# Kernel tuning notes

Measured on AMD Instinct MI355X. Metric: run time of the kernel, lower is better.

## Reference

```python
import jax, jax.numpy as jnp
import numpy as np

N_JOINTS = 18

_RELATIVE_JOINT_MAP = np.array([[0,3,2,1,3,3,3,3,3,3,3,3,3,3,3,3,3,3],[3,0,2,3,1,1,3,3,3,3,2,3,2,2,2,3,3,3],[2,2,0,1,1,3,3,3,1,2,2,3,3,3,3,3,3,3],[1,3,1,0,2,3,3,3,2,3,3,3,3,3,3,3,3,3],[3,1,1,2,0,2,3,2,2,3,1,3,3,3,3,3,3,3],[3,1,3,3,2,0,3,3,3,3,3,3,1,1,1,3,3,3],[3,3,3,3,3,3,0,3,2,1,3,3,3,3,3,3,3,3],[3,3,3,3,2,3,3,0,2,3,1,1,3,3,3,2,2,2],[3,3,1,2,2,3,2,2,0,1,1,3,3,3,3,3,3,3],[3,3,2,3,3,3,1,3,1,0,2,3,3,3,3,3,3,3],[3,2,2,3,1,3,3,1,1,2,0,2,3,3,3,3,3,3],[3,3,3,3,3,3,3,1,3,3,2,0,3,3,3,1,1,1],[3,2,3,3,3,1,3,3,3,3,3,3,0,1,2,3,3,3],[3,2,3,3,3,1,3,3,3,3,3,3,1,0,2,3,3,3],[3,2,3,3,3,1,3,3,3,3,3,3,2,2,0,3,3,3],[3,3,3,3,3,3,3,2,3,3,3,1,3,3,3,0,1,2],[3,3,3,3,3,3,3,2,3,3,3,1,3,3,3,1,0,2],[3,3,3,3,3,3,3,2,3,3,3,1,3,3,3,2,2,0]], dtype=np.int32)

DIM = 512
HEADS = 8
DEPTH = DIM // HEADS  # 64
BATCH = 4096


def setup_inputs() -> dict:
    key = jax.random.key(0)
    ks = jax.random.split(key, 10)
    std = 0.02
    return {
        "k": jax.random.normal(ks[0], (BATCH, N_JOINTS, DIM), jnp.float32),
        "v": jax.random.normal(ks[1], (BATCH, N_JOINTS, DIM), jnp.float32),
        "q": jax.random.normal(ks[2], (BATCH, N_JOINTS, DIM), jnp.float32),
        "Wq": jax.random.normal(ks[3], (DIM, DIM), jnp.float32) * (DIM ** -0.5),
        "Wk": jax.random.normal(ks[4], (DIM, DIM), jnp.float32) * (DIM ** -0.5),
        "Wv": jax.random.normal(ks[5], (DIM, DIM), jnp.float32) * (DIM ** -0.5),
        "Wo": jax.random.normal(ks[6], (DIM, DIM), jnp.float32) * (DIM ** -0.5),
        "bo": jnp.zeros((DIM,), jnp.float32),
        "rel_k": jax.random.normal(ks[7], (4, DEPTH), jnp.float32) * std,
        "rel_v": jax.random.normal(ks[8], (4, DEPTH), jnp.float32) * std,
        "joint_map": jnp.asarray(_RELATIVE_JOINT_MAP),
    }


def reference(k, v, q, Wq, Wk, Wv, Wo, bo, rel_k, rel_v, joint_map):
    B, n, dim = q.shape
    h, d = HEADS, DEPTH
    scale = d ** -0.5

    def split_heads(x):  # [B, n, h*d] -> [B, h, n, d]
        return x.reshape(B, n, h, d).transpose(0, 2, 1, 3)

    qh = split_heads(q @ Wq)
    kh = split_heads(k @ Wk)
    vh = split_heads(v @ Wv)

    # gather relative position tables: [n, n, d]
    r_pos_k = rel_k[joint_map]
    r_pos_v = rel_v[joint_map]

    # relative bias sums over heads AND depth of K (faithful to original einsum)
    rel_bias = jnp.einsum('bhid,ijd->bij', kh, r_pos_k)  # [B, n, n]
    dots = (jnp.einsum('bhid,bhjd->bhij', qh, kh) + rel_bias[:, None, :, :]) * scale
    att = jax.nn.softmax(dots, axis=-1)  # [B, h, n, n]

    out = jnp.einsum('bhij,bhjd->bhid', att, vh) + jnp.einsum('bhij,ijd->bhid', att, r_pos_v)
    out = out.transpose(0, 2, 1, 3).reshape(B, n, dim)
    out = out @ Wo + bo
    return out, att
```

## Files before the change

kernel.cpp:

```cpp
#include <hip/hip_runtime.h>
#include <stdint.h>

#define BATCH 4096
#define NJ 18
#define DIMM 512
#define HEADS 8
#define DEPTH 64
#define MROWS (BATCH*NJ)
#define ATT_OFF ((size_t)MROWS*DIMM)

typedef float f32x4 __attribute__((ext_vector_type(4)));
typedef _Float16 f16_t;
typedef _Float16 f16x8 __attribute__((ext_vector_type(8)));

__device__ __forceinline__ void gl_lds16(const unsigned int* g, unsigned int* l) {
    __builtin_amdgcn_global_load_lds(g, l, 16, 0, 0);
}

__global__ __launch_bounds__(256) void convert_w_kernel(
    const float* __restrict__ W0, const float* __restrict__ W1,
    const float* __restrict__ W2, const float* __restrict__ W3,
    f16_t* __restrict__ T0, f16_t* __restrict__ T1,
    f16_t* __restrict__ T2, f16_t* __restrict__ T3)
{
    const float* W = blockIdx.z == 0 ? W0 : blockIdx.z == 1 ? W1 : blockIdx.z == 2 ? W2 : W3;
    f16_t* T       = blockIdx.z == 0 ? T0 : blockIdx.z == 1 ? T1 : blockIdx.z == 2 ? T2 : T3;
    __shared__ float ld[64][65];
    int k0 = blockIdx.y * 64, n0 = blockIdx.x * 64;
    int tid = threadIdx.x;
    #pragma unroll
    for (int it = 0; it < 16; ++it) {
        int idx = tid + it * 256;
        int kk = idx >> 6, nn = idx & 63;
        ld[kk][nn] = W[(size_t)(k0 + kk) * DIMM + n0 + nn];
    }
    __syncthreads();
    f16x8* T8 = (f16x8*)T;
    #pragma unroll
    for (int it = 0; it < 2; ++it) {
        int c = tid + it * 256;
        int nn = c >> 3, c8 = c & 7;
        int n = n0 + nn, k = k0 + c8 * 8;
        f16x8 val;
        #pragma unroll
        for (int e = 0; e < 8; ++e) val[e] = (f16_t)ld[c8 * 8 + e][nn];
        size_t vi = (size_t)((n >> 7) * 8 + (k >> 6)) * 1024
                  + (n & 127) * 8 + (((k >> 3) & 7) ^ (n & 7));
        T8[vi] = val;
    }
}

template <int MODE>
__global__ __launch_bounds__(256) void gemm16_kernel(
    const void* __restrict__ A0, const void* __restrict__ A1,
    const void* __restrict__ A2,
    const f16_t* __restrict__ B0, const f16_t* __restrict__ B1,
    const f16_t* __restrict__ B2,
    void* __restrict__ C0, void* __restrict__ C1, void* __restrict__ C2,
    const float* __restrict__ bias)
{
    const void* Aparm = blockIdx.z == 0 ? A0 : blockIdx.z == 1 ? A1 : A2;
    const f16_t* Bt   = blockIdx.z == 0 ? B0 : blockIdx.z == 1 ? B1 : B2;
    void* Cparm       = blockIdx.z == 0 ? C0 : blockIdx.z == 1 ? C1 : C2;

    const int p = blockIdx.x + 4 * blockIdx.y;
    const int logical = (p & 7) * (2304 / 8) + (p >> 3);
    const int bn = (logical & 3) * 128;
    const int bm = (logical >> 2) * 128;

    __shared__ __align__(16) f16_t As[MODE == 0 ? 128 * 72 : 128 * 64];
    __shared__ __align__(16) f16_t Bs[128 * 64];

    const int tid = threadIdx.x;
    const int lane = tid & 63;
    const int wv = tid >> 6;
    const int wm = wv >> 1, wn = wv & 1;
    const int l15 = lane & 15, lg = lane >> 4;
    const int swz = (l15 & 7) << 4;
    const int koffb[2] = { (lg * 16) ^ swz, (lg * 16 + 64) ^ swz };

    f32x4 acc[4][4] = {};

    for (int ks = 0; ks < 8; ++ks) {
        __syncthreads();
        {
            const unsigned int* btile =
                (const unsigned int*)(Bt + (size_t)((bn >> 7) * 8 + ks) * 8192);
            unsigned int* bs = (unsigned int*)Bs;
            #pragma unroll
            for (int it = 0; it < 4; ++it) {
                int chunk = wv * 4 + it;
                gl_lds16(btile + chunk * 256 + lane * 4, bs + chunk * 256);
            }
        }
        if constexpr (MODE == 0) {
            const float* A = (const float*)Aparm;
            #pragma unroll
            for (int r = 0; r < 4; ++r) {
                int c = tid + r * 256;
                int row = c >> 3, kc = c & 7;
                const f32x4* p4 = (const f32x4*)(A + (size_t)(bm + row) * DIMM + ks * 64 + kc * 8);
                f32x4 a0 = p4[0], a1 = p4[1];
                f16x8 val;
                val[0] = (f16_t)a0[0]; val[1] = (f16_t)a0[1];
                val[2] = (f16_t)a0[2]; val[3] = (f16_t)a0[3];
                val[4] = (f16_t)a1[0]; val[5] = (f16_t)a1[1];
                val[6] = (f16_t)a1[2]; val[7] = (f16_t)a1[3];
                *(f16x8*)(&As[row * 72 + kc * 8]) = val;
            }
        } else {
            const unsigned int* atile =
                (const unsigned int*)((const f16_t*)Aparm + (size_t)((bm >> 7) * 8 + ks) * 8192);
            unsigned int* as = (unsigned int*)As;
            #pragma unroll
            for (int it = 0; it < 4; ++it) {
                int chunk = wv * 4 + it;
                gl_lds16(atile + chunk * 256 + lane * 4, as + chunk * 256);
            }
        }
        __syncthreads();

        #pragma unroll
        for (int kk = 0; kk < 2; ++kk) {
            const int koff = koffb[kk];
            f16x8 af[4], bfr[4];
            #pragma unroll
            for (int mi = 0; mi < 4; ++mi) {
                int row = wm * 64 + mi * 16 + l15;
                if constexpr (MODE == 0)
                    af[mi] = *(const f16x8*)(&As[row * 72 + kk * 32 + lg * 8]);
                else
                    af[mi] = *(const f16x8*)((const char*)As + row * 128 + koff);
            }
            #pragma unroll
            for (int ni = 0; ni < 4; ++ni) {
                int row = wn * 64 + ni * 16 + l15;
                bfr[ni] = *(const f16x8*)((const char*)Bs + row * 128 + koff);
            }
            #pragma unroll
            for (int mi = 0; mi < 4; ++mi)
                #pragma unroll
                for (int ni = 0; ni < 4; ++ni)
                    acc[mi][ni] = __builtin_amdgcn_mfma_f32_16x16x32_f16(
                        af[mi], bfr[ni], acc[mi][ni], 0, 0, 0);
        }
    }

    #pragma unroll
    for (int mi = 0; mi < 4; ++mi) {
        #pragma unroll
        for (int ni = 0; ni < 4; ++ni) {
            int col = bn + wn * 64 + ni * 16 + l15;
            int rowb = bm + wm * 64 + mi * 16 + lg * 4;
            f32x4 v = acc[mi][ni];
            if constexpr (MODE == 1) {
                float* C = (float*)Cparm;
                float bv = bias[col];
                #pragma unroll
                for (int r = 0; r < 4; ++r)
                    C[(size_t)(rowb + r) * DIMM + col] = v[r] + bv;
            } else {
                f16_t* C = (f16_t*)Cparm;
                #pragma unroll
                for (int r = 0; r < 4; ++r)
                    C[(size_t)(rowb + r) * DIMM + col] = (f16_t)v[r];
            }
        }
    }
}

__global__ __launch_bounds__(256, 3) void attn_kernel(
    const f16_t* __restrict__ qh, const f16_t* __restrict__ kh,
    const f16_t* __restrict__ vh,
    const float* __restrict__ rel_k, const float* __restrict__ rel_v,
    const int* __restrict__ jmap,
    float* __restrict__ att_out, f16_t* __restrict__ ao)
{
    const int b = blockIdx.x;
    const int tid = threadIdx.x;
    __shared__ __align__(16) f16_t k_s[NJ * DIMM];
    __shared__ __align__(16) f16_t v_s[NJ * DIMM];
    __shared__ float relk_s[4 * DEPTH];
    __shared__ float relv_s[4 * DEPTH];
    __shared__ int map_s[NJ * NJ];
    __shared__ float ksum_s[NJ * DEPTH];
    __shared__ float t4_s[NJ * 4];

    const size_t base = (size_t)b * (NJ * DIMM);
    const uint4* kg = (const uint4*)(kh + base);
    const uint4* vg = (const uint4*)(vh + base);
    uint4* ks4 = (uint4*)k_s;
    uint4* vs4 = (uint4*)v_s;
    for (int c = tid; c < 2 * NJ * 64; c += 256) {
        int t = c / (NJ * 64);
        int e = c - t * (NJ * 64);
        int m = e & 63;
        int pos = (e & ~63) + (m & 56) + (((m & 7) + (m >> 3)) & 7);
        uint4 val = (t == 0 ? kg : vg)[e];
        (t == 0 ? ks4 : vs4)[pos] = val;
    }
    relk_s[tid & 255] = rel_k[tid & 255];
    relv_s[tid & 255] = rel_v[tid & 255];
    for (int e = tid; e < NJ * NJ; e += 256) map_s[e] = jmap[e];

    const int h = tid / NJ, i = tid - (tid / NJ) * NJ;
    const bool act = tid < HEADS * NJ;
    f16x8 qr[8];
    if (act) {
        const f16x8* qp = (const f16x8*)(qh + base + i * DIMM + h * DEPTH);
        #pragma unroll
        for (int t = 0; t < 8; ++t) qr[t] = qp[t];
    }
    __syncthreads();

    const f16x8* ks8 = (const f16x8*)k_s;
    const f16x8* vs8 = (const f16x8*)v_s;

    for (int e = tid; e < NJ * DEPTH; e += 256) {
        int ii = e >> 6, dd = e & 63;
        int tt = dd >> 3, d7 = dd & 7;
        float s = 0.f;
        #pragma unroll
        for (int hh = 0; hh < HEADS; ++hh)
            s += (float)k_s[((ii << 6) + (hh << 3) + ((tt + hh) & 7)) * 8 + d7];
        ksum_s[e] = s;
    }
    __syncthreads();
    if (tid < NJ * 4) {
        int ii = tid >> 2, c = tid & 3;
        float s = 0.f;
        #pragma unroll
        for (int dd = 0; dd < DEPTH; ++dd)
            s += ksum_s[ii * DEPTH + dd] * relk_s[c * DEPTH + dd];
        t4_s[tid] = s;
    }
    __syncthreads();

    if (!act) return;

    float att[NJ];
    float m = -1e30f;
    #pragma unroll
    for (int j = 0; j < NJ; ++j) {
        float s = 0.f;
        #pragma unroll
        for (int t = 0; t < 8; ++t) {
            f16x8 kv = ks8[(j << 6) + (h << 3) + ((t + h) & 7)];
            f16x8 a = qr[t];
            #pragma unroll
            for (int e = 0; e < 8; ++e) s += (float)a[e] * (float)kv[e];
        }
        s += t4_s[i * 4 + map_s[i * NJ + j]];
        s *= 0.125f;
        att[j] = s;
        m = fmaxf(m, s);
    }
    float sum = 0.f;
    #pragma unroll
    for (int j = 0; j < NJ; ++j) { att[j] = __expf(att[j] - m); sum += att[j]; }
    const float inv = 1.f / sum;
    float s4[4] = {0.f, 0.f, 0.f, 0.f};
    float* ap = att_out + (((size_t)b * HEADS + h) * NJ + i) * NJ;
    #pragma unroll
    for (int j = 0; j < NJ; ++j) {
        float a = att[j] * inv;
        att[j] = a;
        ap[j] = a;
        int c = map_s[i * NJ + j];
        s4[0] += (c == 0) ? a : 0.f;
        s4[1] += (c == 1) ? a : 0.f;
        s4[2] += (c == 2) ? a : 0.f;
        s4[3] += (c == 3) ? a : 0.f;
    }

    const size_t grow = (size_t)b * NJ + i;
    f16x8* aot = (f16x8*)ao + ((grow >> 7) * 8 + h) * 1024 + (grow & 127) * 8;
    const int rr7 = (int)(grow & 7);
    #pragma unroll
    for (int half = 0; half < 2; ++half) {
        float acc[32] = {};
        #pragma unroll
        for (int j = 0; j < NJ; ++j) {
            float a = att[j];
            #pragma unroll
            for (int t = 0; t < 4; ++t) {
                int tt = half * 4 + t;
                f16x8 vv = vs8[(j << 6) + (h << 3) + ((tt + h) & 7)];
                #pragma unroll
                for (int e = 0; e < 8; ++e) acc[t * 8 + e] += a * (float)vv[e];
            }
        }
        #pragma unroll
        for (int c = 0; c < 4; ++c) {
            float sc = s4[c];
            #pragma unroll
            for (int d = 0; d < 32; ++d)
                acc[d] += sc * relv_s[c * DEPTH + half * 32 + d];
        }
        #pragma unroll
        for (int t = 0; t < 4; ++t) {
            f16x8 res;
            #pragma unroll
            for (int e = 0; e < 8; ++e) res[e] = (f16_t)acc[t * 8 + e];
            aot[(half * 4 + t) ^ rr7] = res;
        }
    }
}

extern "C" void kernel_launch(void* const* d_in, const int* in_sizes, int n_in,
                              void* d_out, int out_size, void* d_ws, size_t ws_size,
                              hipStream_t stream) {
    (void)in_sizes; (void)n_in; (void)out_size; (void)ws_size;
    const float* k_in = (const float*)d_in[0];
    const float* v_in = (const float*)d_in[1];
    const float* q_in = (const float*)d_in[2];
    const float* Wq   = (const float*)d_in[3];
    const float* Wk   = (const float*)d_in[4];
    const float* Wv   = (const float*)d_in[5];
    const float* Wo   = (const float*)d_in[6];
    const float* bo   = (const float*)d_in[7];
    const float* relk = (const float*)d_in[8];
    const float* relv = (const float*)d_in[9];
    const int*   jmap = (const int*)d_in[10];

    char* ws = (char*)d_ws;
    const size_t WT = (size_t)DIMM * DIMM * sizeof(f16_t);
    f16_t* Tq = (f16_t*)(ws + 0 * WT);
    f16_t* Tk = (f16_t*)(ws + 1 * WT);
    f16_t* Tv = (f16_t*)(ws + 2 * WT);
    f16_t* To = (f16_t*)(ws + 3 * WT);
    const size_t PSZ = (size_t)MROWS * DIMM * sizeof(f16_t);
    f16_t* qh = (f16_t*)(ws + 4 * WT + 0 * PSZ);
    f16_t* kh = (f16_t*)(ws + 4 * WT + 1 * PSZ);
    f16_t* vh = (f16_t*)(ws + 4 * WT + 2 * PSZ);
    f16_t* ao = (f16_t*)(ws + 4 * WT + 3 * PSZ);

    float* outp = (float*)d_out;
    float* attp = outp + ATT_OFF;

    convert_w_kernel<<<dim3(8, 8, 4), 256, 0, stream>>>(
        Wq, Wk, Wv, Wo, Tq, Tk, Tv, To);

    gemm16_kernel<0><<<dim3(DIMM / 128, MROWS / 128, 3), 256, 0, stream>>>(
        q_in, k_in, v_in, Tq, Tk, Tv, qh, kh, vh, nullptr);

    attn_kernel<<<BATCH, 256, 0, stream>>>(qh, kh, vh, relk, relv, jmap, attp, ao);

    gemm16_kernel<1><<<dim3(DIMM / 128, MROWS / 128, 1), 256, 0, stream>>>(
        ao, nullptr, nullptr, To, nullptr, nullptr, outp, nullptr, nullptr, bo);
}
```

Measured before the change: 447.8 us.

## Double-buffer B tile in LDS and load A fragments directly into registers

The GEMM kernel drops the A shared-memory tile. Each wave now loads its A fragments straight from global memory into registers, converting fp32 to fp16 in registers for MODE 0 or reading the pre-swizzled fp16 image for MODE 1. The B tile is double-buffered in LDS, and the next k-step is prefetched with global_load_lds before the current MFMAs run, using hand-placed vmcnt waits and barriers. The aim is to overlap global loads with compute and cut LDS traffic and one barrier per k-step. In exchange it relies on fragile hand-counted vmcnt values and on uncoalesced per-lane A reads in MODE 0, where the second half of each A step is loaded late without prefetch.

```diff
diff --git a/kernel.cpp b/kernel.cpp
--- a/kernel.cpp
+++ b/kernel.cpp
@@ -68,8 +68,7 @@
     const int bn = (logical & 3) * 128;
     const int bm = (logical >> 2) * 128;
 
-    __shared__ __align__(16) f16_t As[MODE == 0 ? 128 * 72 : 128 * 64];
-    __shared__ __align__(16) f16_t Bs[128 * 64];
+    __shared__ __align__(16) f16_t Bs[2][128 * 64];
 
     const int tid = threadIdx.x;
     const int lane = tid & 63;
@@ -79,63 +78,91 @@
     const int swz = (l15 & 7) << 4;
     const int koffb[2] = { (lg * 16) ^ swz, (lg * 16 + 64) ^ swz };
 
+    const float* arow = (const float*)Aparm
+        + (size_t)(bm + wm * 64 + l15) * DIMM + lg * 8;
+    const f16x8* aimg = (const f16x8*)Aparm
+        + (size_t)(bm >> 7) * 8 * 1024 + (wm * 64 + l15) * 8;
+    const int axor = l15 & 7;
+
     f32x4 acc[4][4] = {};
 
+    auto stageB = [&](int ks, int buf) {
+        const unsigned int* btile =
+            (const unsigned int*)(Bt + (size_t)((bn >> 7) * 8 + ks) * 8192);
+        unsigned int* bs = (unsigned int*)(&Bs[buf][0]);
+        #pragma unroll
+        for (int it = 0; it < 4; ++it) {
+            int chunk = wv * 4 + it;
+            gl_lds16(btile + chunk * 256 + lane * 4, bs + chunk * 256);
+        }
+    };
+
+    stageB(0, 0);
+
     for (int ks = 0; ks < 8; ++ks) {
-        __syncthreads();
-        {
-            const unsigned int* btile =
-                (const unsigned int*)(Bt + (size_t)((bn >> 7) * 8 + ks) * 8192);
-            unsigned int* bs = (unsigned int*)Bs;
-            #pragma unroll
-            for (int it = 0; it < 4; ++it) {
-                int chunk = wv * 4 + it;
-                gl_lds16(btile + chunk * 256 + lane * 4, bs + chunk * 256);
-            }
-        }
+        const int buf = ks & 1;
+
+        f32x4 a0p[4], a1p[4];
+        f16x8 afp[8];
         if constexpr (MODE == 0) {
-            const float* A = (const float*)Aparm;
-            #pragma unroll
-            for (int r = 0; r < 4; ++r) {
-                int c = tid + r * 256;
-                int row = c >> 3, kc = c & 7;
-                const f32x4* p4 = (const f32x4*)(A + (size_t)(bm + row) * DIMM + ks * 64 + kc * 8);
-                f32x4 a0 = p4[0], a1 = p4[1];
-                f16x8 val;
-                val[0] = (f16_t)a0[0]; val[1] = (f16_t)a0[1];
-                val[2] = (f16_t)a0[2]; val[3] = (f16_t)a0[3];
-                val[4] = (f16_t)a1[0]; val[5] = (f16_t)a1[1];
-                val[6] = (f16_t)a1[2]; val[7] = (f16_t)a1[3];
-                *(f16x8*)(&As[row * 72 + kc * 8]) = val;
+            #pragma unroll
+            for (int mi = 0; mi < 4; ++mi) {
+                const f32x4* ap = (const f32x4*)(arow + (size_t)mi * 16 * DIMM + ks * 64);
+                a0p[mi] = ap[0];
+                a1p[mi] = ap[1];
             }
         } else {
-            const unsigned int* atile =
-                (const unsigned int*)((const f16_t*)Aparm + (size_t)((bm >> 7) * 8 + ks) * 8192);
-            unsigned int* as = (unsigned int*)As;
-            #pragma unroll
-            for (int it = 0; it < 4; ++it) {
-                int chunk = wv * 4 + it;
-                gl_lds16(atile + chunk * 256 + lane * 4, as + chunk * 256);
-            }
-        }
-        __syncthreads();
+            #pragma unroll
+            for (int kk = 0; kk < 2; ++kk)
+                #pragma unroll
+                for (int mi = 0; mi < 4; ++mi)
+                    afp[kk * 4 + mi] = aimg[ks * 1024 + mi * 128 + ((kk * 4 + lg) ^ axor)];
+        }
+
+        if (ks < 7) stageB(ks + 1, buf ^ 1);
+
+        if (ks < 7) asm volatile("s_waitcnt vmcnt(12)" ::: "memory");
+        else        asm volatile("s_waitcnt vmcnt(8)"  ::: "memory");
+        __builtin_amdgcn_s_barrier();
+        __builtin_amdgcn_sched_barrier(0);
 
         #pragma unroll
         for (int kk = 0; kk < 2; ++kk) {
             const int koff = koffb[kk];
             f16x8 af[4], bfr[4];
-            #pragma unroll
-            for (int mi = 0; mi < 4; ++mi) {
-                int row = wm * 64 + mi * 16 + l15;
-                if constexpr (MODE == 0)
-                    af[mi] = *(const f16x8*)(&As[row * 72 + kk * 32 + lg * 8]);
-                else
-                    af[mi] = *(const f16x8*)((const char*)As + row * 128 + koff);
+            if constexpr (MODE == 0) {
+                if (kk == 0) {
+                    #pragma unroll
+                    for (int mi = 0; mi < 4; ++mi) {
+                        f32x4 a0 = a0p[mi], a1 = a1p[mi];
+                        f16x8 v;
+                        v[0] = (f16_t)a0[0]; v[1] = (f16_t)a0[1];
+                        v[2] = (f16_t)a0[2]; v[3] = (f16_t)a0[3];
+                        v[4] = (f16_t)a1[0]; v[5] = (f16_t)a1[1];
+                        v[6] = (f16_t)a1[2]; v[7] = (f16_t)a1[3];
+                        af[mi] = v;
+                    }
+                } else {
+                    #pragma unroll
+                    for (int mi = 0; mi < 4; ++mi) {
+                        const f32x4* ap = (const f32x4*)(arow + (size_t)mi * 16 * DIMM + ks * 64 + 32);
+                        f32x4 a0 = ap[0], a1 = ap[1];
+                        f16x8 v;
+                        v[0] = (f16_t)a0[0]; v[1] = (f16_t)a0[1];
+                        v[2] = (f16_t)a0[2]; v[3] = (f16_t)a0[3];
+                        v[4] = (f16_t)a1[0]; v[5] = (f16_t)a1[1];
+                        v[6] = (f16_t)a1[2]; v[7] = (f16_t)a1[3];
+                        af[mi] = v;
+                    }
+                }
+            } else {
+                #pragma unroll
+                for (int mi = 0; mi < 4; ++mi) af[mi] = afp[kk * 4 + mi];
             }
             #pragma unroll
             for (int ni = 0; ni < 4; ++ni) {
                 int row = wn * 64 + ni * 16 + l15;
-                bfr[ni] = *(const f16x8*)((const char*)Bs + row * 128 + koff);
+                bfr[ni] = *(const f16x8*)((const char*)(&Bs[buf][0]) + row * 128 + koff);
             }
             #pragma unroll
             for (int mi = 0; mi < 4; ++mi)
@@ -144,6 +171,9 @@
                     acc[mi][ni] = __builtin_amdgcn_mfma_f32_16x16x32_f16(
                         af[mi], bfr[ni], acc[mi][ni], 0, 0, 0);
         }
+
+        asm volatile("s_waitcnt lgkmcnt(0)" ::: "memory");
+        __builtin_amdgcn_s_barrier();
     }
 
     #pragma unroll
```

New measurement: 714.9 us. 59.6% more time.

## Software-pipeline fp32 A loads and double-buffer B tiles in QKV GEMM

Applied to the files above, without the earlier changes.

In the MODE 0 GEMM (fp32 activations converted to fp16), the loop now issues the next k-step's A register loads and B global-to-LDS copies before computing on the current step. B lives in a double-buffered LDS array, and synchronisation uses manual waitcnt plus scheduling barriers. The goal is to hide global memory latency behind the MFMA work. The cost is more registers for prefetched A, twice the LDS for B, and hand-tuned waitcnt counts that must match the number of outstanding loads. MODE 1 behaves as before.

```diff
diff --git a/kernel.cpp b/kernel.cpp
--- a/kernel.cpp
+++ b/kernel.cpp
@@ -16,6 +16,9 @@
 __device__ __forceinline__ void gl_lds16(const unsigned int* g, unsigned int* l) {
     __builtin_amdgcn_global_load_lds(g, l, 16, 0, 0);
 }
+#define SBAR()  do { __builtin_amdgcn_sched_barrier(0); \
+                     __builtin_amdgcn_s_barrier();      \
+                     __builtin_amdgcn_sched_barrier(0); } while (0)
 
 __global__ __launch_bounds__(256) void convert_w_kernel(
     const float* __restrict__ W0, const float* __restrict__ W1,
@@ -69,7 +72,7 @@
     const int bm = (logical >> 2) * 128;
 
     __shared__ __align__(16) f16_t As[MODE == 0 ? 128 * 72 : 128 * 64];
-    __shared__ __align__(16) f16_t Bs[128 * 64];
+    __shared__ __align__(16) f16_t Bs[MODE == 0 ? 2 * 128 * 64 : 128 * 64];
 
     const int tid = threadIdx.x;
     const int lane = tid & 63;
@@ -81,68 +84,128 @@
 
     f32x4 acc[4][4] = {};
 
-    for (int ks = 0; ks < 8; ++ks) {
-        __syncthreads();
-        {
-            const unsigned int* btile =
-                (const unsigned int*)(Bt + (size_t)((bn >> 7) * 8 + ks) * 8192);
-            unsigned int* bs = (unsigned int*)Bs;
-            #pragma unroll
-            for (int it = 0; it < 4; ++it) {
-                int chunk = wv * 4 + it;
-                gl_lds16(btile + chunk * 256 + lane * 4, bs + chunk * 256);
-            }
-        }
-        if constexpr (MODE == 0) {
-            const float* A = (const float*)Aparm;
+    auto stageB = [&](int ks, int buf) {
+        const unsigned int* btile =
+            (const unsigned int*)(Bt + (size_t)((bn >> 7) * 8 + ks) * 8192);
+        unsigned int* bs = (unsigned int*)(&Bs[0]) + buf * 4096;
+        #pragma unroll
+        for (int it = 0; it < 4; ++it) {
+            int chunk = wv * 4 + it;
+            gl_lds16(btile + chunk * 256 + lane * 4, bs + chunk * 256);
+        }
+    };
+
+    if constexpr (MODE == 0) {
+        const int kc = tid & 7;
+        const int rw0 = tid >> 3;
+        const float* abase[4];
+        #pragma unroll
+        for (int r = 0; r < 4; ++r)
+            abase[r] = (const float*)Aparm + (size_t)(bm + rw0 + r * 32) * DIMM + kc * 8;
+
+        f32x4 apre[8];
+        #pragma unroll
+        for (int r = 0; r < 4; ++r) {
+            const f32x4* ap = (const f32x4*)(abase[r]);
+            apre[r * 2]     = ap[0];
+            apre[r * 2 + 1] = ap[1];
+        }
+        stageB(0, 0);
+
+        #pragma unroll
+        for (int ks = 0; ks < 8; ++ks) {
+            const int buf = ks & 1;
+
+            f16x8 vals[4];
             #pragma unroll
             for (int r = 0; r < 4; ++r) {
-                int c = tid + r * 256;
-                int row = c >> 3, kc = c & 7;
-                const f32x4* p4 = (const f32x4*)(A + (size_t)(bm + row) * DIMM + ks * 64 + kc * 8);
-                f32x4 a0 = p4[0], a1 = p4[1];
-                f16x8 val;
-                val[0] = (f16_t)a0[0]; val[1] = (f16_t)a0[1];
-                val[2] = (f16_t)a0[2]; val[3] = (f16_t)a0[3];
-                val[4] = (f16_t)a1[0]; val[5] = (f16_t)a1[1];
-                val[6] = (f16_t)a1[2]; val[7] = (f16_t)a1[3];
-                *(f16x8*)(&As[row * 72 + kc * 8]) = val;
-            }
-        } else {
-            const unsigned int* atile =
-                (const unsigned int*)((const f16_t*)Aparm + (size_t)((bm >> 7) * 8 + ks) * 8192);
-            unsigned int* as = (unsigned int*)As;
-            #pragma unroll
-            for (int it = 0; it < 4; ++it) {
-                int chunk = wv * 4 + it;
-                gl_lds16(atile + chunk * 256 + lane * 4, as + chunk * 256);
-            }
-        }
-        __syncthreads();
-
-        #pragma unroll
-        for (int kk = 0; kk < 2; ++kk) {
-            const int koff = koffb[kk];
-            f16x8 af[4], bfr[4];
-            #pragma unroll
-            for (int mi = 0; mi < 4; ++mi) {
-                int row = wm * 64 + mi * 16 + l15;
-                if constexpr (MODE == 0)
+                f32x4 a0 = apre[r * 2], a1 = apre[r * 2 + 1];
+                f16x8 v;
+                v[0] = (f16_t)a0[0]; v[1] = (f16_t)a0[1];
+                v[2] = (f16_t)a0[2]; v[3] = (f16_t)a0[3];
+                v[4] = (f16_t)a1[0]; v[5] = (f16_t)a1[1];
+                v[6] = (f16_t)a1[2]; v[7] = (f16_t)a1[3];
+                vals[r] = v;
+            }
+            #pragma unroll
+            for (int r = 0; r < 4; ++r)
+                *(f16x8*)(&As[(rw0 + r * 32) * 72 + kc * 8]) = vals[r];
+
+            if (ks < 7) {
+                #pragma unroll
+                for (int r = 0; r < 4; ++r) {
+                    const f32x4* ap = (const f32x4*)(abase[r] + (ks + 1) * 64);
+                    apre[r * 2]     = ap[0];
+                    apre[r * 2 + 1] = ap[1];
+                }
+                stageB(ks + 1, buf ^ 1);
+                asm volatile("s_waitcnt vmcnt(12) lgkmcnt(0)" ::: "memory");
+            } else {
+                asm volatile("s_waitcnt vmcnt(0) lgkmcnt(0)" ::: "memory");
+            }
+            SBAR();
+
+            #pragma unroll
+            for (int kk = 0; kk < 2; ++kk) {
+                const int koff = koffb[kk];
+                f16x8 af[4], bfr[4];
+                #pragma unroll
+                for (int mi = 0; mi < 4; ++mi) {
+                    int row = wm * 64 + mi * 16 + l15;
                     af[mi] = *(const f16x8*)(&As[row * 72 + kk * 32 + lg * 8]);
-                else
+                }
+                #pragma unroll
+                for (int ni = 0; ni < 4; ++ni) {
+                    int row = wn * 64 + ni * 16 + l15;
+                    bfr[ni] = *(const f16x8*)((const char*)(&Bs[0]) + buf * 16384 + row * 128 + koff);
+                }
+                #pragma unroll
+                for (int mi = 0; mi < 4; ++mi)
+                    #pragma unroll
+                    for (int ni = 0; ni < 4; ++ni)
+                        acc[mi][ni] = __builtin_amdgcn_mfma_f32_16x16x32_f16(
+                            af[mi], bfr[ni], acc[mi][ni], 0, 0, 0);
+            }
+
+            asm volatile("s_waitcnt lgkmcnt(0)" ::: "memory");
+            SBAR();
+        }
+    } else {
+        for (int ks = 0; ks < 8; ++ks) {
+            __syncthreads();
+            stageB(ks, 0);
+            {
+                const unsigned int* atile =
+                    (const unsigned int*)((const f16_t*)Aparm + (size_t)((bm >> 7) * 8 + ks) * 8192);
+                unsigned int* as = (unsigned int*)As;
+                #pragma unroll
+                for (int it = 0; it < 4; ++it) {
+                    int chunk = wv * 4 + it;
+                    gl_lds16(atile + chunk * 256 + lane * 4, as + chunk * 256);
+                }
+            }
+            __syncthreads();
+            #pragma unroll
+            for (int kk = 0; kk < 2; ++kk) {
+                const int koff = koffb[kk];
+                f16x8 af[4], bfr[4];
+                #pragma unroll
+                for (int mi = 0; mi < 4; ++mi) {
+                    int row = wm * 64 + mi * 16 + l15;
                     af[mi] = *(const f16x8*)((const char*)As + row * 128 + koff);
-            }
-            #pragma unroll
-            for (int ni = 0; ni < 4; ++ni) {
-                int row = wn * 64 + ni * 16 + l15;
-                bfr[ni] = *(const f16x8*)((const char*)Bs + row * 128 + koff);
-            }
-            #pragma unroll
-            for (int mi = 0; mi < 4; ++mi)
-                #pragma unroll
-                for (int ni = 0; ni < 4; ++ni)
-                    acc[mi][ni] = __builtin_amdgcn_mfma_f32_16x16x32_f16(
-                        af[mi], bfr[ni], acc[mi][ni], 0, 0, 0);
+                }
+                #pragma unroll
+                for (int ni = 0; ni < 4; ++ni) {
+                    int row = wn * 64 + ni * 16 + l15;
+                    bfr[ni] = *(const f16x8*)((const char*)(&Bs[0]) + row * 128 + koff);
+                }
+                #pragma unroll
+                for (int mi = 0; mi < 4; ++mi)
+                    #pragma unroll
+                    for (int ni = 0; ni < 4; ++ni)
+                        acc[mi][ni] = __builtin_amdgcn_mfma_f32_16x16x32_f16(
+                            af[mi], bfr[ni], acc[mi][ni], 0, 0, 0);
+            }
         }
     }
 
```

New measurement: 471.4 us. 1.05x slower.
